# Performance work log

Measured on AMD Instinct MI355X. Metric: run time of the kernel, lower is better.

The kernel has to match this reference:

```python
import jax, jax.numpy as jnp
import numpy as np

B = 1024
IN_H, IN_W = 128, 128
KH, KW = 10, 10
SH, SW = 5, 5
PH, PW = 2, 2
HP, WP = IN_H + 2 * PH, IN_W + 2 * PW          # padded dims: 132, 132
NKH = (IN_H - KH + 2 * PH) // SH + 1            # 25
NKW = (IN_W - KW + 2 * PW) // SW + 1            # 25
NK = NKH * NKW                                  # 625


def _build_weight_matrix(kernel_weights):
    """kernel_weights: [NK, KH, KW] -> sparse-structured dense [HP*WP, NK].
    Faithful to LocallyConnected2dV2._create_weight_matrix, vectorized."""
    i = jnp.arange(NK)
    start_i = (i // NKW) * SH                   # [NK]
    start_j = (i % NKW) * SW                    # [NK]
    # flat row index for each (kernel, k, l) tap in padded image
    rows = ((start_i[:, None, None] + jnp.arange(KH)[None, :, None]) * WP
            + start_j[:, None, None] + jnp.arange(KW)[None, None, :])  # [NK,KH,KW]
    rows = rows.reshape(NK, KH * KW)
    cols = i[:, None]                           # [NK,1] broadcasts over taps
    W = jnp.zeros((HP * WP, NK), dtype=kernel_weights.dtype)
    return W.at[rows, cols].set(kernel_weights.reshape(NK, KH * KW))


def setup_inputs() -> dict:
    key = jax.random.key(0)
    kx, kw, kb = jax.random.split(key, 3)
    x = jax.random.normal(kx, (B, IN_H, IN_W), dtype=jnp.float32)
    kernel_weights = jax.random.normal(kw, (NK, KH, KW), dtype=jnp.float32)
    W = _build_weight_matrix(kernel_weights)    # [HP*WP, NK]
    bias = jax.random.normal(kb, (NKH, NKW), dtype=jnp.float32)
    return {"x": x, "W": W, "bias": bias}


def reference(x, W, bias):
    # zero-pad spatial dims, flatten, dense GEMM against sparse-structured W
    xp = jnp.pad(x, ((0, 0), (PH, PH), (PW, PW)))          # [B,HP,WP]
    xf = xp.reshape(x.shape[0], HP * WP)                   # [B,HP*WP]
    out = xf @ W                                           # [B,NK]
    out = out.reshape(x.shape[0], NKH, NKW)
    return out + bias
```

## Files before the change

### kernel.cpp

```cpp
#include <hip/hip_runtime.h>

typedef _Float16 f16x2 __attribute__((ext_vector_type(2)));
typedef __fp16  fp16x2 __attribute__((ext_vector_type(2)));

constexpr int NKW  = 25, NK = 625;
constexpr int WPADR = 132;
constexpr int WPT   = 160;
constexpr int RST   = 35;

union U2H { unsigned int u; f16x2 h; fp16x2 p; };

__global__ void gather_wp(const float* __restrict__ W, _Float16* __restrict__ wgpT) {
    int t = blockIdx.x * 256 + threadIdx.x;
    if (t >= NK * WPT) return;
    int k = t / WPT, p = t % WPT;
    int di = p >> 4, s = p & 15;
    int ki = k / NKW, kj = k % NKW;
    int o = (5 * kj + 2) & 3;
    int j = s - o;
    float val = 0.f;
    if (j >= 0 && j < 10)
        val = W[(size_t)((ki * 5 + di) * WPADR + kj * 5 + j) * NK + k];
    wgpT[((size_t)(p >> 3) * NK + k) * 8 + (p & 7)] = (_Float16)val;
}

__device__ __forceinline__ float dot2acc(unsigned int a, unsigned int b, float c) {
    U2H ua, ub; ua.u = a; ub.u = b;
#if __has_builtin(__builtin_amdgcn_fdot2)
    return __builtin_amdgcn_fdot2(ua.h, ub.h, c, false);
#else
    return c + (float)ua.h.x * (float)ub.h.x + (float)ua.h.y * (float)ub.h.y;
#endif
}

template <bool USE_WG>
__global__ __launch_bounds__(256, 2)
void lc2d_img(const float* __restrict__ x, const _Float16* __restrict__ wgpT,
              const float* __restrict__ Wfull,
              const float* __restrict__ bias, float* __restrict__ out) {
    __shared__ uint2 xs[70 * RST];

    const int b    = blockIdx.x;
    const int half = blockIdx.y;
    const int P0   = half ? 65 : 0;
    const int NR   = half ? 65 : 70;
    const int K0   = half ? 13 : 0;
    const int NOUT = half ? 300 : 325;
    const int tid  = threadIdx.x;

    for (int i = tid; i < NR * 2; i += 256)
        xs[(i >> 1) * RST + (i & 1) * 33] = make_uint2(0u, 0u);

    const float* xb = x + ((size_t)b << 14);
    for (int i = tid; i < NR * 32; i += 256) {
        const int idx = i >> 5, q = (i & 31) + 1;
        const int r = P0 + idx - 2;
        uint2 val = make_uint2(0u, 0u);
        if (r >= 0 && r < 128) {
            const float4 v = *reinterpret_cast<const float4*>(xb + (r << 7) + ((q - 1) << 2));
            U2H u0, u1;
            u0.p = __builtin_amdgcn_cvt_pkrtz(v.x, v.y);
            u1.p = __builtin_amdgcn_cvt_pkrtz(v.z, v.w);
            val.x = u0.u; val.y = u1.u;
        }
        xs[idx * RST + q] = val;
    }
    __syncthreads();

    const uint4* wt4 = reinterpret_cast<const uint4*>(wgpT);

    for (int k_local = tid; k_local < NOUT; k_local += 256) {
        const int k    = K0 * NKW + k_local;
        const int ki_l = k_local / 25;
        const int kj   = k_local - ki_l * 25;
        const uint2* base = xs + ki_l * 5 * RST + ((5 * kj + 2) >> 2);

        uint4 wq[20];
        if (USE_WG) {
#pragma unroll
            for (int j = 0; j < 20; ++j) wq[j] = wt4[(size_t)j * NK + k];
        } else {
            const int o = (5 * kj + 2) & 3;
#pragma unroll
            for (int j = 0; j < 20; ++j) {
                const int di = j >> 1, pb = (j & 1) * 8;
                unsigned int uu[4];
#pragma unroll
                for (int m = 0; m < 4; ++m) {
                    float f0 = 0.f, f1 = 0.f;
                    const int j0 = pb + 2 * m - o, j1 = pb + 2 * m + 1 - o;
                    const size_t rowb = (size_t)(((K0 + ki_l) * 5 + di) * WPADR + kj * 5);
                    if (j0 >= 0 && j0 < 10) f0 = Wfull[(rowb + j0) * NK + k];
                    if (j1 >= 0 && j1 < 10) f1 = Wfull[(rowb + j1) * NK + k];
                    U2H u; u.p = __builtin_amdgcn_cvt_pkrtz(f0, f1);
                    uu[m] = u.u;
                }
                wq[j] = make_uint4(uu[0], uu[1], uu[2], uu[3]);
            }
        }

        float acc0 = bias[k], acc1 = 0.f;
#pragma unroll
        for (int d = 0; d < 10; ++d) {
            const uint2* rowp = base + d * RST;
            const uint2 a0 = rowp[0], a1 = rowp[1], a2 = rowp[2], a3 = rowp[3];
            const uint4 wA = wq[2 * d], wB = wq[2 * d + 1];
            acc0 = dot2acc(a0.x, wA.x, acc0);
            acc1 = dot2acc(a0.y, wA.y, acc1);
            acc0 = dot2acc(a1.x, wA.z, acc0);
            acc1 = dot2acc(a1.y, wA.w, acc1);
            acc0 = dot2acc(a2.x, wB.x, acc0);
            acc1 = dot2acc(a2.y, wB.y, acc1);
            acc0 = dot2acc(a3.x, wB.z, acc0);
            acc1 = dot2acc(a3.y, wB.w, acc1);
        }
        out[(size_t)b * NK + k] = acc0 + acc1;
    }
}

extern "C" void kernel_launch(void* const* d_in, const int* in_sizes, int n_in,
                              void* d_out, int out_size, void* d_ws, size_t ws_size,
                              hipStream_t stream) {
    const float* x    = (const float*)d_in[0];
    const float* W    = (const float*)d_in[1];
    const float* bias = (const float*)d_in[2];
    float* out = (float*)d_out;

    const dim3 grid(1024, 2);
    if (ws_size >= (size_t)NK * WPT * sizeof(_Float16)) {
        _Float16* wgpT = (_Float16*)d_ws;
        gather_wp<<<(NK * WPT + 255) / 256, 256, 0, stream>>>(W, wgpT);
        lc2d_img<true><<<grid, 256, 0, stream>>>(x, wgpT, W, bias, out);
    } else {
        lc2d_img<false><<<grid, 256, 0, stream>>>(x, nullptr, W, bias, out);
    }
}
```

Before: 127.8 us.

## Process two images per block with output-row quarters to reuse weights in registers

Each block now handles a pair of images and a quarter of the output rows (6–7 kernel rows), so every thread owns exactly one output column. Its fp16 weight taps are loaded into registers once and used for both images. Both images' padded row slices are staged in shared memory before a single barrier. The aim is to halve per-image weight traffic and remove the output loop, at the cost of more shared memory per block, idle threads in blocks with only 150 outputs, and a higher occupancy target.

```diff
diff --git a/kernel.cpp b/kernel.cpp
--- a/kernel.cpp
+++ b/kernel.cpp
@@ -7,6 +7,7 @@
 constexpr int WPADR = 132;
 constexpr int WPT   = 160;
 constexpr int RST   = 35;
+constexpr int MAXR  = 40;
 
 union U2H { unsigned int u; f16x2 h; fp16x2 p; };
 
@@ -34,49 +35,30 @@
 }
 
 template <bool USE_WG>
-__global__ __launch_bounds__(256, 2)
-void lc2d_img(const float* __restrict__ x, const _Float16* __restrict__ wgpT,
-              const float* __restrict__ Wfull,
-              const float* __restrict__ bias, float* __restrict__ out) {
-    __shared__ uint2 xs[70 * RST];
+__global__ __launch_bounds__(256, 3)
+void lc2d_pair(const float* __restrict__ x, const _Float16* __restrict__ wgpT,
+               const float* __restrict__ Wfull,
+               const float* __restrict__ bias, float* __restrict__ out) {
+    __shared__ uint2 xs[2 * MAXR * RST];
 
-    const int b    = blockIdx.x;
-    const int half = blockIdx.y;
-    const int P0   = half ? 65 : 0;
-    const int NR   = half ? 65 : 70;
-    const int K0   = half ? 13 : 0;
-    const int NOUT = half ? 300 : 325;
+    const int pair    = blockIdx.x;
+    const int quarter = blockIdx.y;
+    const int K0   = quarter ? (1 + 6 * quarter) : 0;
+    const int NKI  = quarter ? 6 : 7;
+    const int NROWS = 5 * NKI + 5;
+    const int NOUT  = NKI * NKW;
     const int tid  = threadIdx.x;
 
-    for (int i = tid; i < NR * 2; i += 256)
-        xs[(i >> 1) * RST + (i & 1) * 33] = make_uint2(0u, 0u);
+    const bool active = tid < NOUT;
+    const int ki_l = tid / 25;
+    const int kj   = tid - ki_l * 25;
+    const int k    = (K0 + ki_l) * NKW + kj;
 
-    const float* xb = x + ((size_t)b << 14);
-    for (int i = tid; i < NR * 32; i += 256) {
-        const int idx = i >> 5, q = (i & 31) + 1;
-        const int r = P0 + idx - 2;
-        uint2 val = make_uint2(0u, 0u);
-        if (r >= 0 && r < 128) {
-            const float4 v = *reinterpret_cast<const float4*>(xb + (r << 7) + ((q - 1) << 2));
-            U2H u0, u1;
-            u0.p = __builtin_amdgcn_cvt_pkrtz(v.x, v.y);
-            u1.p = __builtin_amdgcn_cvt_pkrtz(v.z, v.w);
-            val.x = u0.u; val.y = u1.u;
-        }
-        xs[idx * RST + q] = val;
-    }
-    __syncthreads();
-
-    const uint4* wt4 = reinterpret_cast<const uint4*>(wgpT);
-
-    for (int k_local = tid; k_local < NOUT; k_local += 256) {
-        const int k    = K0 * NKW + k_local;
-        const int ki_l = k_local / 25;
-        const int kj   = k_local - ki_l * 25;
-        const uint2* base = xs + ki_l * 5 * RST + ((5 * kj + 2) >> 2);
-
-        uint4 wq[20];
+    uint4 wq[20];
+    float bval = 0.f;
+    if (active) {
         if (USE_WG) {
+            const uint4* wt4 = reinterpret_cast<const uint4*>(wgpT);
 #pragma unroll
             for (int j = 0; j < 20; ++j) wq[j] = wt4[(size_t)j * NK + k];
         } else {
@@ -98,8 +80,39 @@
                 wq[j] = make_uint4(uu[0], uu[1], uu[2], uu[3]);
             }
         }
+        bval = bias[k];
+    }
 
-        float acc0 = bias[k], acc1 = 0.f;
+#pragma unroll
+    for (int img = 0; img < 2; ++img) {
+        const float* xb = x + ((size_t)(2 * pair + img) << 14);
+        uint2* xd = xs + img * (MAXR * RST);
+        for (int i = tid; i < NROWS * 2; i += 256)
+            xd[(i >> 1) * RST + (i & 1) * 33] = make_uint2(0u, 0u);
+        for (int i = tid; i < NROWS * 32; i += 256) {
+            const int idx = i >> 5, q = (i & 31) + 1;
+            const int r = 5 * K0 + idx - 2;
+            uint2 val = make_uint2(0u, 0u);
+            if (r >= 0 && r < 128) {
+                const float4 v = *reinterpret_cast<const float4*>(
+                    xb + (r << 7) + ((q - 1) << 2));
+                U2H u0, u1;
+                u0.p = __builtin_amdgcn_cvt_pkrtz(v.x, v.y);
+                u1.p = __builtin_amdgcn_cvt_pkrtz(v.z, v.w);
+                val.x = u0.u; val.y = u1.u;
+            }
+            xd[idx * RST + q] = val;
+        }
+    }
+    __syncthreads();
+
+    if (!active) return;
+
+    const int woff = (5 * kj + 2) >> 2;
+#pragma unroll
+    for (int img = 0; img < 2; ++img) {
+        const uint2* base = xs + img * (MAXR * RST) + (5 * ki_l) * RST + woff;
+        float acc0 = bval, acc1 = 0.f;
 #pragma unroll
         for (int d = 0; d < 10; ++d) {
             const uint2* rowp = base + d * RST;
@@ -114,7 +127,7 @@
             acc0 = dot2acc(a3.x, wB.z, acc0);
             acc1 = dot2acc(a3.y, wB.w, acc1);
         }
-        out[(size_t)b * NK + k] = acc0 + acc1;
+        out[(size_t)(2 * pair + img) * NK + k] = acc0 + acc1;
     }
 }
 
@@ -126,12 +139,12 @@
     const float* bias = (const float*)d_in[2];
     float* out = (float*)d_out;
 
-    const dim3 grid(1024, 2);
+    const dim3 grid(512, 4);
     if (ws_size >= (size_t)NK * WPT * sizeof(_Float16)) {
         _Float16* wgpT = (_Float16*)d_ws;
         gather_wp<<<(NK * WPT + 255) / 256, 256, 0, stream>>>(W, wgpT);
-        lc2d_img<true><<<grid, 256, 0, stream>>>(x, wgpT, W, bias, out);
+        lc2d_pair<true><<<grid, 256, 0, stream>>>(x, wgpT, W, bias, out);
     } else {
-        lc2d_img<false><<<grid, 256, 0, stream>>>(x, nullptr, W, bias, out);
+        lc2d_pair<false><<<grid, 256, 0, stream>>>(x, nullptr, W, bias, out);
     }
 }
```

New measurement: 131.7 us. 3.0% more time.
